# Kernel tuning notes

Measured on AMD Instinct MI355X. Metric: run time of the kernel, lower is better.

## Reference

```python
import jax, jax.numpy as jnp
import numpy as np

N, F, A = 50000, 128, 128

def setup_inputs() -> dict:
    key = jax.random.key(0)
    ks = jax.random.split(key, 20)
    r = lambda i, shape: jax.random.normal(ks[i], shape, dtype=jnp.float32)
    w = lambda i, shape: jax.random.normal(ks[i], shape, dtype=jnp.float32) * 0.05
    return {
        "feat": r(0, (N, F)),
        "mu": r(1, (N, F, 3)),
        "T0": r(2, (N,)),
        "T1": r(3, (N, 3)),
        "T2": r(4, (N, 3, 3)),
        "T3": r(5, (N, 3, 3, 3)),
        # denseq: Dense(F,F,swish) -> Dense(F,F). Weights stored [in,out].
        "Wq1": w(6, (F, F)), "bq1": jnp.zeros((F,), jnp.float32),
        "Wq2": w(7, (F, F)), "bq2": jnp.zeros((F,), jnp.float32),
        "WT1": w(8, (F, F)),  # dense_T1, no bias
        "WT2": w(9, (F, F)),  # dense_T2, no bias
        "WT3": w(10, (F, F)), # dense_T3, no bias
        # dense_s: Dense(F,F,swish) -> Dense(F,A)
        "Ws1": w(11, (F, F)), "bs1": jnp.zeros((F,), jnp.float32),
        "Ws2": w(12, (F, A)), "bs2": jnp.zeros((A,), jnp.float32),
        "Wv": w(13, (F, A)),  # dense_v, no bias
    }

def reference(feat, mu, T0, T1, T2, T3,
              Wq1, bq1, Wq2, bq2, WT1, WT2, WT3,
              Ws1, bs1, Ws2, bs2, Wv):
    silu = jax.nn.silu  # swish
    # M0 = denseq(feat): [N, F]
    M0 = silu(feat @ Wq1 + bq1) @ Wq2 + bq2
    # M1/M2/M3: linear over feature dim of mu [N, F, 3]
    M1 = jnp.einsum('nfc,fg->ngc', mu, WT1)
    M2 = jnp.einsum('nfc,fg->ngc', mu, WT2)
    M3 = jnp.einsum('nfc,fg->ngc', mu, WT3)
    # scalar channel
    ms = jnp.sum(M1 * T1[:, None, :], axis=-1) + T0[:, None] * M0          # T1, T0 terms
    ms = ms + jnp.einsum('nfi,nfj,nij->nf', M2, M2, T2)                    # quadrupole . T2
    ms = ms + jnp.einsum('nfi,nfj,nfk,nijk->nf', M3, M3, M3, T3)           # octupole . T3
    # vector channel [N, F, 3]
    mv = T1[:, None, :] * M0[..., None]
    mv = mv + jnp.einsum('nij,nfj->nfi', T2, M1)
    mv = mv + jnp.einsum('nijk,nfj,nfk->nfi', T3, M2, M2)
    # output projections
    mv_out = jnp.einsum('nfc,fa->nac', mv, Wv)                             # [N, A, 3]
    ms_out = silu(ms @ Ws1 + bs1) @ Ws2 + bs2                              # [N, A]
    return ms_out, mv_out
```

## Files before the change

### kernel.cpp

```cpp
#include <hip/hip_runtime.h>
#include <cstdint>

#define N_NODES 50000
#define TILE 32
#define NBLK ((N_NODES + TILE - 1) / TILE)

typedef __bf16 bf16x8 __attribute__((ext_vector_type(8)));
typedef unsigned short ushort8_t __attribute__((ext_vector_type(8)));
typedef float f32x4 __attribute__((ext_vector_type(4)));

__device__ __forceinline__ unsigned short f2bf(float x) {
  union { float f; uint32_t u; } v; v.f = x;
  uint32_t r = v.u + 0x7FFFu + ((v.u >> 16) & 1u);
  return (unsigned short)(r >> 16);
}

__device__ __forceinline__ float fast_silu(float x) {
  return x / (1.0f + __expf(-x));
}

__global__ __launch_bounds__(256) void prep_weights(
    const float* __restrict__ Wq1, const float* __restrict__ Wq2,
    const float* __restrict__ WT1, const float* __restrict__ WT2,
    const float* __restrict__ WT3, const float* __restrict__ Ws1,
    const float* __restrict__ Ws2, const float* __restrict__ Wv,
    unsigned short* __restrict__ ws) {
  int tid = blockIdx.x * 256 + threadIdx.x;
  int w = tid >> 11;
  int rest = tid & 2047;
  int c = rest >> 8;
  int kt = (rest >> 6) & 3;
  int lane = rest & 63;
  int g = (lane & 15) + 16 * c;
  int k0 = kt * 32 + (lane >> 4) * 8;
  const float* srcs[8] = {Wq1, Wq2, WT1, WT2, WT3, Ws1, Ws2, Wv};
  const float* src = srcs[w];
  union { unsigned short u[8]; uint4 v; } o;
#pragma unroll
  for (int j = 0; j < 8; ++j) o.u[j] = f2bf(src[(k0 + j) * 128 + g]);
  *(uint4*)(ws + (size_t)w * 16384 + (size_t)rest * 8) = o.v;
}

__device__ __forceinline__ bf16x8 ldB(const unsigned short* __restrict__ wg,
                                      int c, int kt, int lane) {
  return __builtin_bit_cast(
      bf16x8, *(const ushort8_t*)(wg + (((c * 4 + kt) * 64 + lane)) * 8));
}

__device__ __forceinline__ bf16x8 ldA(const unsigned short* __restrict__ sA,
                                      int row, int k0) {
  return __builtin_bit_cast(bf16x8, *(const ushort8_t*)(sA + row * 136 + k0));
}

__device__ __forceinline__ void gemm16g(const unsigned short* __restrict__ sA,
                                        const unsigned short* __restrict__ wg,
                                        int lane, int cb, f32x4 acc[2][2]) {
  const int m = lane & 15, q = lane >> 4;
  bf16x8 b[2][4], a0[4], a1[4];
#pragma unroll
  for (int cc = 0; cc < 2; ++cc)
#pragma unroll
    for (int kt = 0; kt < 4; ++kt) b[cc][kt] = ldB(wg, cb + cc, kt, lane);
#pragma unroll
  for (int kt = 0; kt < 4; ++kt) {
    const int k0 = q * 8 + kt * 32;
    a0[kt] = ldA(sA, m, k0);
    a1[kt] = ldA(sA, m + 16, k0);
  }
  const f32x4 vzero = {0.f, 0.f, 0.f, 0.f};
#pragma unroll
  for (int rt = 0; rt < 2; ++rt)
#pragma unroll
    for (int cc = 0; cc < 2; ++cc) acc[rt][cc] = vzero;
#pragma unroll
  for (int kt = 0; kt < 4; ++kt)
#pragma unroll
    for (int cc = 0; cc < 2; ++cc) {
      acc[0][cc] = __builtin_amdgcn_mfma_f32_16x16x32_bf16(a0[kt], b[cc][kt], acc[0][cc], 0, 0, 0);
      acc[1][cc] = __builtin_amdgcn_mfma_f32_16x16x32_bf16(a1[kt], b[cc][kt], acc[1][cc], 0, 0, 0);
    }
}

__device__ __forceinline__ void gemm3g(const unsigned short* __restrict__ s0,
                                       const unsigned short* __restrict__ s1,
                                       const unsigned short* __restrict__ s2,
                                       const unsigned short* __restrict__ wg,
                                       int lane, int cb,
                                       f32x4 A1[2][2], f32x4 A2[2][2],
                                       f32x4 A3[2][2]) {
  const int m = lane & 15, q = lane >> 4;
  bf16x8 b[2][4];
#pragma unroll
  for (int cc = 0; cc < 2; ++cc)
#pragma unroll
    for (int kt = 0; kt < 4; ++kt) b[cc][kt] = ldB(wg, cb + cc, kt, lane);
  const f32x4 vzero = {0.f, 0.f, 0.f, 0.f};
#pragma unroll
  for (int rt = 0; rt < 2; ++rt)
#pragma unroll
    for (int cc = 0; cc < 2; ++cc) {
      A1[rt][cc] = vzero; A2[rt][cc] = vzero; A3[rt][cc] = vzero;
    }
#pragma unroll
  for (int kt = 0; kt < 4; ++kt) {
    const int k0 = q * 8 + kt * 32;
    bf16x8 a00 = ldA(s0, m, k0);
    bf16x8 a01 = ldA(s0, m + 16, k0);
    bf16x8 a10 = ldA(s1, m, k0);
    bf16x8 a11 = ldA(s1, m + 16, k0);
    bf16x8 a20 = ldA(s2, m, k0);
    bf16x8 a21 = ldA(s2, m + 16, k0);
#pragma unroll
    for (int cc = 0; cc < 2; ++cc) {
      A1[0][cc] = __builtin_amdgcn_mfma_f32_16x16x32_bf16(a00, b[cc][kt], A1[0][cc], 0, 0, 0);
      A1[1][cc] = __builtin_amdgcn_mfma_f32_16x16x32_bf16(a01, b[cc][kt], A1[1][cc], 0, 0, 0);
      A2[0][cc] = __builtin_amdgcn_mfma_f32_16x16x32_bf16(a10, b[cc][kt], A2[0][cc], 0, 0, 0);
      A2[1][cc] = __builtin_amdgcn_mfma_f32_16x16x32_bf16(a11, b[cc][kt], A2[1][cc], 0, 0, 0);
      A3[0][cc] = __builtin_amdgcn_mfma_f32_16x16x32_bf16(a20, b[cc][kt], A3[0][cc], 0, 0, 0);
      A3[1][cc] = __builtin_amdgcn_mfma_f32_16x16x32_bf16(a21, b[cc][kt], A3[1][cc], 0, 0, 0);
    }
  }
}

__global__ __launch_bounds__(256, 2) void multipole_main(
    const float* __restrict__ feat, const float* __restrict__ mu,
    const float* __restrict__ T0g, const float* __restrict__ T1g,
    const float* __restrict__ T2g, const float* __restrict__ T3g,
    const float* __restrict__ bq1, const float* __restrict__ bq2,
    const float* __restrict__ bs1, const float* __restrict__ bs2,
    const unsigned short* __restrict__ ws, float* __restrict__ out) {
  __shared__ unsigned short sXmain[TILE * 136];
  __shared__ unsigned short sXmu[3][TILE * 136];
  __shared__ float sT[TILE][47];

  const int t = threadIdx.x;
  const int lane = t & 63, wv = t >> 6;
  const int m = lane & 15, q = lane >> 4;
  const int cb = wv * 2;
  const int nodeBase = blockIdx.x * TILE;

  {
    int node = t >> 3, f0 = (t & 7) * 16;
    int gn = nodeBase + node;
    union { unsigned short u[16]; uint4 v[2]; } buf;
    if (gn < N_NODES) {
      const f32x4* p = (const f32x4*)(feat + (size_t)gn * 128 + f0);
      float xs[16];
#pragma unroll
      for (int i = 0; i < 4; ++i) *(f32x4*)(xs + 4 * i) = __builtin_nontemporal_load(p + i);
#pragma unroll
      for (int i = 0; i < 16; ++i) buf.u[i] = f2bf(xs[i]);
    } else {
#pragma unroll
      for (int i = 0; i < 16; ++i) buf.u[i] = 0;
    }
    uint4* dst = (uint4*)&sXmain[node * 136 + f0];
    dst[0] = buf.v[0]; dst[1] = buf.v[1];
  }

  {
    int node = t >> 3, f0 = (t & 7) * 16;
    int gn = nodeBase + node;
    union { unsigned short u[16]; uint4 v[2]; } b3[3];
    if (gn < N_NODES) {
      const f32x4* p = (const f32x4*)(mu + ((size_t)gn * 128 + f0) * 3);
      float xs[48];
#pragma unroll
      for (int i = 0; i < 12; ++i) *(f32x4*)(xs + 4 * i) = __builtin_nontemporal_load(p + i);
#pragma unroll
      for (int i = 0; i < 16; ++i) {
        b3[0].u[i] = f2bf(xs[i * 3 + 0]);
        b3[1].u[i] = f2bf(xs[i * 3 + 1]);
        b3[2].u[i] = f2bf(xs[i * 3 + 2]);
      }
    } else {
#pragma unroll
      for (int ch = 0; ch < 3; ++ch)
#pragma unroll
        for (int i = 0; i < 16; ++i) b3[ch].u[i] = 0;
    }
#pragma unroll
    for (int ch = 0; ch < 3; ++ch) {
      uint4* dst = (uint4*)&sXmu[ch][node * 136 + f0];
      dst[0] = b3[ch].v[0]; dst[1] = b3[ch].v[1];
    }
  }

  if (t < TILE) {
    int n = nodeBase + t;
    bool val = n < N_NODES;
    float t0 = val ? __builtin_nontemporal_load(T0g + n) : 0.f;
    float t1[3], t2[9], t3[27];
#pragma unroll
    for (int i = 0; i < 3; ++i) t1[i] = val ? __builtin_nontemporal_load(T1g + n * 3 + i) : 0.f;
#pragma unroll
    for (int i = 0; i < 9; ++i) t2[i] = val ? __builtin_nontemporal_load(T2g + n * 9 + i) : 0.f;
#pragma unroll
    for (int i = 0; i < 27; ++i) t3[i] = val ? __builtin_nontemporal_load(T3g + n * 27 + i) : 0.f;
    float* Tr = sT[t];
    Tr[0] = t0;
    Tr[1] = t1[0]; Tr[2] = t1[1]; Tr[3] = t1[2];
#pragma unroll
    for (int i = 0; i < 9; ++i) Tr[4 + i] = t2[i];
    Tr[13] = t2[0]; Tr[14] = t2[1] + t2[3]; Tr[15] = t2[2] + t2[6];
    Tr[16] = t2[4]; Tr[17] = t2[5] + t2[7]; Tr[18] = t2[8];
    Tr[19] = t3[0];
    Tr[20] = t3[1] + t3[3] + t3[9];
    Tr[21] = t3[2] + t3[6] + t3[18];
    Tr[22] = t3[4] + t3[10] + t3[12];
    Tr[23] = t3[5] + t3[7] + t3[11] + t3[15] + t3[19] + t3[21];
    Tr[24] = t3[8] + t3[20] + t3[24];
    Tr[25] = t3[13];
    Tr[26] = t3[14] + t3[16] + t3[22];
    Tr[27] = t3[17] + t3[23] + t3[25];
    Tr[28] = t3[26];
#pragma unroll
    for (int i = 0; i < 3; ++i) {
      const float* b = t3 + 9 * i;
      float* d = Tr + 29 + 6 * i;
      d[0] = b[0]; d[1] = b[1] + b[3]; d[2] = b[2] + b[6];
      d[3] = b[4]; d[4] = b[5] + b[7]; d[5] = b[8];
    }
  }
  __syncthreads();

  f32x4 A1[2][2], A2[2][2], A3[2][2];
  float msv[2][2][4];
  float mvv[3][2][2][4];

  gemm16g(sXmain, ws, lane, cb, A1);
  float b0 = bq1[cb * 16 + m], b1 = bq1[cb * 16 + 16 + m];
  __syncthreads();
#pragma unroll
  for (int rt = 0; rt < 2; ++rt)
#pragma unroll
    for (int ri = 0; ri < 4; ++ri) {
      int lrow = rt * 16 + q * 4 + ri;
#pragma unroll
      for (int cc = 0; cc < 2; ++cc) {
        float h = fast_silu(A1[rt][cc][ri] + (cc ? b1 : b0));
        sXmain[lrow * 136 + (cb + cc) * 16 + m] = f2bf(h);
      }
    }
  __syncthreads();

  gemm16g(sXmain, ws + 1 * 16384, lane, cb, A1);
  {
    float bb0 = bq2[cb * 16 + m], bb1 = bq2[cb * 16 + 16 + m];
#pragma unroll
    for (int rt = 0; rt < 2; ++rt)
#pragma unroll
      for (int ri = 0; ri < 4; ++ri) {
        const float* Tr = sT[rt * 16 + q * 4 + ri];
        float t0 = Tr[0], ta = Tr[1], tb = Tr[2], tc = Tr[3];
#pragma unroll
        for (int cc = 0; cc < 2; ++cc) {
          float m0 = A1[rt][cc][ri] + (cc ? bb1 : bb0);
          msv[rt][cc][ri] = t0 * m0;
          mvv[0][rt][cc][ri] = ta * m0;
          mvv[1][rt][cc][ri] = tb * m0;
          mvv[2][rt][cc][ri] = tc * m0;
        }
      }
  }

  gemm3g(sXmu[0], sXmu[1], sXmu[2], ws + 2 * 16384, lane, cb, A1, A2, A3);
#pragma unroll
  for (int rt = 0; rt < 2; ++rt)
#pragma unroll
    for (int ri = 0; ri < 4; ++ri) {
      const float* Tr = sT[rt * 16 + q * 4 + ri];
#pragma unroll
      for (int cc = 0; cc < 2; ++cc) {
        float v0 = A1[rt][cc][ri], v1 = A2[rt][cc][ri], v2 = A3[rt][cc][ri];
        msv[rt][cc][ri] += Tr[1] * v0 + Tr[2] * v1 + Tr[3] * v2;
        mvv[0][rt][cc][ri] += Tr[4] * v0 + Tr[5] * v1 + Tr[6] * v2;
        mvv[1][rt][cc][ri] += Tr[7] * v0 + Tr[8] * v1 + Tr[9] * v2;
        mvv[2][rt][cc][ri] += Tr[10] * v0 + Tr[11] * v1 + Tr[12] * v2;
      }
    }

  gemm3g(sXmu[0], sXmu[1], sXmu[2], ws + 4 * 16384, lane, cb, A1, A2, A3);
#pragma unroll
  for (int rt = 0; rt < 2; ++rt)
#pragma unroll
    for (int ri = 0; ri < 4; ++ri) {
      const float* Cp = sT[rt * 16 + q * 4 + ri] + 19;
      float c0 = Cp[0], c1 = Cp[1], c2 = Cp[2], c3 = Cp[3], c4 = Cp[4];
      float c5 = Cp[5], c6 = Cp[6], c7 = Cp[7], c8 = Cp[8], c9 = Cp[9];
#pragma unroll
      for (int cc = 0; cc < 2; ++cc) {
        float u0 = A1[rt][cc][ri], u1 = A2[rt][cc][ri], u2 = A3[rt][cc][ri];
        float Q0 = u0 * u0, Q1 = u0 * u1, Q2 = u0 * u2;
        float Q3 = u1 * u1, Q4 = u1 * u2, Q5 = u2 * u2;
        msv[rt][cc][ri] += c0 * (Q0 * u0) + c1 * (Q0 * u1) + c2 * (Q0 * u2) +
                           c3 * (Q1 * u1) + c4 * (Q1 * u2) + c5 * (Q2 * u2) +
                           c6 * (Q3 * u1) + c7 * (Q3 * u2) + c8 * (Q4 * u2) +
                           c9 * (Q5 * u2);
      }
    }

  gemm3g(sXmu[0], sXmu[1], sXmu[2], ws + 3 * 16384, lane, cb, A1, A2, A3);
#pragma unroll
  for (int rt = 0; rt < 2; ++rt)
#pragma unroll
    for (int ri = 0; ri < 4; ++ri) {
      const float* Tr = sT[rt * 16 + q * 4 + ri];
      const float* q2 = Tr + 13;
      const float* d3 = Tr + 29;
      float q20 = q2[0], q21 = q2[1], q22 = q2[2], q23 = q2[3], q24 = q2[4], q25 = q2[5];
#pragma unroll
      for (int cc = 0; cc < 2; ++cc) {
        float v0 = A1[rt][cc][ri], v1 = A2[rt][cc][ri], v2 = A3[rt][cc][ri];
        float P0 = v0 * v0, P1 = v0 * v1, P2 = v0 * v2;
        float P3 = v1 * v1, P4 = v1 * v2, P5 = v2 * v2;
        msv[rt][cc][ri] += q20 * P0 + q21 * P1 + q22 * P2 + q23 * P3 + q24 * P4 + q25 * P5;
        mvv[0][rt][cc][ri] += d3[0] * P0 + d3[1] * P1 + d3[2] * P2 + d3[3] * P3 + d3[4] * P4 + d3[5] * P5;
        mvv[1][rt][cc][ri] += d3[6] * P0 + d3[7] * P1 + d3[8] * P2 + d3[9] * P3 + d3[10] * P4 + d3[11] * P5;
        mvv[2][rt][cc][ri] += d3[12] * P0 + d3[13] * P1 + d3[14] * P2 + d3[15] * P3 + d3[16] * P4 + d3[17] * P5;
      }
    }
  __syncthreads();

#pragma unroll
  for (int rt = 0; rt < 2; ++rt)
#pragma unroll
    for (int ri = 0; ri < 4; ++ri) {
      int lrow = rt * 16 + q * 4 + ri;
#pragma unroll
      for (int cc = 0; cc < 2; ++cc) {
        int col = (cb + cc) * 16 + m;
        sXmain[lrow * 136 + col] = f2bf(msv[rt][cc][ri]);
        sXmu[0][lrow * 136 + col] = f2bf(mvv[0][rt][cc][ri]);
        sXmu[1][lrow * 136 + col] = f2bf(mvv[1][rt][cc][ri]);
        sXmu[2][lrow * 136 + col] = f2bf(mvv[2][rt][cc][ri]);
      }
    }
  __syncthreads();

  gemm16g(sXmain, ws + 5 * 16384, lane, cb, A1);
  {
    float s0 = bs1[cb * 16 + m], s1 = bs1[cb * 16 + 16 + m];
    __syncthreads();
#pragma unroll
    for (int rt = 0; rt < 2; ++rt)
#pragma unroll
      for (int ri = 0; ri < 4; ++ri) {
        int lrow = rt * 16 + q * 4 + ri;
#pragma unroll
        for (int cc = 0; cc < 2; ++cc) {
          float g = fast_silu(A1[rt][cc][ri] + (cc ? s1 : s0));
          sXmain[lrow * 136 + (cb + cc) * 16 + m] = f2bf(g);
        }
      }
  }
  __syncthreads();

  gemm16g(sXmain, ws + 6 * 16384, lane, cb, A1);
  {
    float s0 = bs2[cb * 16 + m], s1 = bs2[cb * 16 + 16 + m];
#pragma unroll
    for (int rt = 0; rt < 2; ++rt)
#pragma unroll
      for (int ri = 0; ri < 4; ++ri) {
        int grow = nodeBase + rt * 16 + q * 4 + ri;
        if (grow < N_NODES) {
#pragma unroll
          for (int cc = 0; cc < 2; ++cc) {
            int col = (cb + cc) * 16 + m;
            __builtin_nontemporal_store(A1[rt][cc][ri] + (cc ? s1 : s0),
                                        out + (size_t)grow * 128 + col);
          }
        }
      }
  }

  float* out2 = out + (size_t)N_NODES * 128;
  gemm3g(sXmu[0], sXmu[1], sXmu[2], ws + 7 * 16384, lane, cb, A1, A2, A3);
#pragma unroll
  for (int rt = 0; rt < 2; ++rt)
#pragma unroll
    for (int ri = 0; ri < 4; ++ri) {
      int grow = nodeBase + rt * 16 + q * 4 + ri;
      if (grow < N_NODES) {
#pragma unroll
        for (int cc = 0; cc < 2; ++cc) {
          int col = (cb + cc) * 16 + m;
          float* p = out2 + ((size_t)grow * 128 + col) * 3;
          __builtin_nontemporal_store(A1[rt][cc][ri], p + 0);
          __builtin_nontemporal_store(A2[rt][cc][ri], p + 1);
          __builtin_nontemporal_store(A3[rt][cc][ri], p + 2);
        }
      }
    }
}

extern "C" void kernel_launch(void* const* d_in, const int* in_sizes, int n_in,
                              void* d_out, int out_size, void* d_ws, size_t ws_size,
                              hipStream_t stream) {
  const float* feat = (const float*)d_in[0];
  const float* mu   = (const float*)d_in[1];
  const float* T0   = (const float*)d_in[2];
  const float* T1   = (const float*)d_in[3];
  const float* T2   = (const float*)d_in[4];
  const float* T3   = (const float*)d_in[5];
  const float* Wq1  = (const float*)d_in[6];
  const float* bq1  = (const float*)d_in[7];
  const float* Wq2  = (const float*)d_in[8];
  const float* bq2  = (const float*)d_in[9];
  const float* WT1  = (const float*)d_in[10];
  const float* WT2  = (const float*)d_in[11];
  const float* WT3  = (const float*)d_in[12];
  const float* Ws1  = (const float*)d_in[13];
  const float* bs1  = (const float*)d_in[14];
  const float* Ws2  = (const float*)d_in[15];
  const float* bs2  = (const float*)d_in[16];
  const float* Wv   = (const float*)d_in[17];
  unsigned short* ws = (unsigned short*)d_ws;
  float* out = (float*)d_out;

  prep_weights<<<64, 256, 0, stream>>>(Wq1, Wq2, WT1, WT2, WT3, Ws1, Ws2, Wv, ws);
  multipole_main<<<NBLK, 256, 0, stream>>>(feat, mu, T0, T1, T2, T3,
                                           bq1, bq2, bs1, bs2, ws, out);
}
```

Before: 300.2 us.

## Prefetch next weight fragments during GEMMs, double-buffer activations, vectorize epilogues

Measured after the change: 306.3 us. 2.0% more time.

```diff
diff --git a/kernel.cpp b/kernel.cpp
--- a/kernel.cpp
+++ b/kernel.cpp
@@ -8,15 +8,18 @@
 typedef __bf16 bf16x8 __attribute__((ext_vector_type(8)));
 typedef unsigned short ushort8_t __attribute__((ext_vector_type(8)));
 typedef float f32x4 __attribute__((ext_vector_type(4)));
+typedef float f32x2 __attribute__((ext_vector_type(2)));
 
 __device__ __forceinline__ unsigned short f2bf(float x) {
-  union { float f; uint32_t u; } v; v.f = x;
-  uint32_t r = v.u + 0x7FFFu + ((v.u >> 16) & 1u);
-  return (unsigned short)(r >> 16);
+  return __builtin_bit_cast(unsigned short, (__bf16)x);
 }
 
 __device__ __forceinline__ float fast_silu(float x) {
   return x / (1.0f + __expf(-x));
+}
+
+__device__ __forceinline__ f32x4 ld4(const float* p) {
+  return *(const f32x4*)p;
 }
 
 __global__ __launch_bounds__(256) void prep_weights(
@@ -47,20 +50,27 @@
       bf16x8, *(const ushort8_t*)(wg + (((c * 4 + kt) * 64 + lane)) * 8));
 }
 
+struct BF { bf16x8 v[2][4]; };
+
+__device__ __forceinline__ BF loadB8(const unsigned short* __restrict__ wg,
+                                     int lane, int cb) {
+  BF r;
+#pragma unroll
+  for (int cc = 0; cc < 2; ++cc)
+#pragma unroll
+    for (int kt = 0; kt < 4; ++kt) r.v[cc][kt] = ldB(wg, cb + cc, kt, lane);
+  return r;
+}
+
 __device__ __forceinline__ bf16x8 ldA(const unsigned short* __restrict__ sA,
                                       int row, int k0) {
   return __builtin_bit_cast(bf16x8, *(const ushort8_t*)(sA + row * 136 + k0));
 }
 
-__device__ __forceinline__ void gemm16g(const unsigned short* __restrict__ sA,
-                                        const unsigned short* __restrict__ wg,
-                                        int lane, int cb, f32x4 acc[2][2]) {
+__device__ __forceinline__ void gemm16p(const unsigned short* __restrict__ sA,
+                                        const BF& B, int lane, f32x4 acc[2][2]) {
   const int m = lane & 15, q = lane >> 4;
-  bf16x8 b[2][4], a0[4], a1[4];
-#pragma unroll
-  for (int cc = 0; cc < 2; ++cc)
-#pragma unroll
-    for (int kt = 0; kt < 4; ++kt) b[cc][kt] = ldB(wg, cb + cc, kt, lane);
+  bf16x8 a0[4], a1[4];
 #pragma unroll
   for (int kt = 0; kt < 4; ++kt) {
     const int k0 = q * 8 + kt * 32;
@@ -76,24 +86,18 @@
   for (int kt = 0; kt < 4; ++kt)
 #pragma unroll
     for (int cc = 0; cc < 2; ++cc) {
-      acc[0][cc] = __builtin_amdgcn_mfma_f32_16x16x32_bf16(a0[kt], b[cc][kt], acc[0][cc], 0, 0, 0);
-      acc[1][cc] = __builtin_amdgcn_mfma_f32_16x16x32_bf16(a1[kt], b[cc][kt], acc[1][cc], 0, 0, 0);
-    }
-}
-
-__device__ __forceinline__ void gemm3g(const unsigned short* __restrict__ s0,
+      acc[0][cc] = __builtin_amdgcn_mfma_f32_16x16x32_bf16(a0[kt], B.v[cc][kt], acc[0][cc], 0, 0, 0);
+      acc[1][cc] = __builtin_amdgcn_mfma_f32_16x16x32_bf16(a1[kt], B.v[cc][kt], acc[1][cc], 0, 0, 0);
+    }
+}
+
+__device__ __forceinline__ void gemm3p(const unsigned short* __restrict__ s0,
                                        const unsigned short* __restrict__ s1,
                                        const unsigned short* __restrict__ s2,
-                                       const unsigned short* __restrict__ wg,
-                                       int lane, int cb,
+                                       const BF& B, int lane,
                                        f32x4 A1[2][2], f32x4 A2[2][2],
                                        f32x4 A3[2][2]) {
   const int m = lane & 15, q = lane >> 4;
-  bf16x8 b[2][4];
-#pragma unroll
-  for (int cc = 0; cc < 2; ++cc)
-#pragma unroll
-    for (int kt = 0; kt < 4; ++kt) b[cc][kt] = ldB(wg, cb + cc, kt, lane);
   const f32x4 vzero = {0.f, 0.f, 0.f, 0.f};
 #pragma unroll
   for (int rt = 0; rt < 2; ++rt)
@@ -112,15 +116,17 @@
     bf16x8 a21 = ldA(s2, m + 16, k0);
 #pragma unroll
     for (int cc = 0; cc < 2; ++cc) {
-      A1[0][cc] = __builtin_amdgcn_mfma_f32_16x16x32_bf16(a00, b[cc][kt], A1[0][cc], 0, 0, 0);
-      A1[1][cc] = __builtin_amdgcn_mfma_f32_16x16x32_bf16(a01, b[cc][kt], A1[1][cc], 0, 0, 0);
-      A2[0][cc] = __builtin_amdgcn_mfma_f32_16x16x32_bf16(a10, b[cc][kt], A2[0][cc], 0, 0, 0);
-      A2[1][cc] = __builtin_amdgcn_mfma_f32_16x16x32_bf16(a11, b[cc][kt], A2[1][cc], 0, 0, 0);
-      A3[0][cc] = __builtin_amdgcn_mfma_f32_16x16x32_bf16(a20, b[cc][kt], A3[0][cc], 0, 0, 0);
-      A3[1][cc] = __builtin_amdgcn_mfma_f32_16x16x32_bf16(a21, b[cc][kt], A3[1][cc], 0, 0, 0);
-    }
-  }
-}
+      A1[0][cc] = __builtin_amdgcn_mfma_f32_16x16x32_bf16(a00, B.v[cc][kt], A1[0][cc], 0, 0, 0);
+      A1[1][cc] = __builtin_amdgcn_mfma_f32_16x16x32_bf16(a01, B.v[cc][kt], A1[1][cc], 0, 0, 0);
+      A2[0][cc] = __builtin_amdgcn_mfma_f32_16x16x32_bf16(a10, B.v[cc][kt], A2[0][cc], 0, 0, 0);
+      A2[1][cc] = __builtin_amdgcn_mfma_f32_16x16x32_bf16(a11, B.v[cc][kt], A2[1][cc], 0, 0, 0);
+      A3[0][cc] = __builtin_amdgcn_mfma_f32_16x16x32_bf16(a20, B.v[cc][kt], A3[0][cc], 0, 0, 0);
+      A3[1][cc] = __builtin_amdgcn_mfma_f32_16x16x32_bf16(a21, B.v[cc][kt], A3[1][cc], 0, 0, 0);
+    }
+  }
+}
+
+#define ST_STRIDE 56
 
 __global__ __launch_bounds__(256, 2) void multipole_main(
     const float* __restrict__ feat, const float* __restrict__ mu,
@@ -130,14 +136,20 @@
     const float* __restrict__ bs1, const float* __restrict__ bs2,
     const unsigned short* __restrict__ ws, float* __restrict__ out) {
   __shared__ unsigned short sXmain[TILE * 136];
+  __shared__ unsigned short sXmain2[TILE * 136];
   __shared__ unsigned short sXmu[3][TILE * 136];
-  __shared__ float sT[TILE][47];
+  __shared__ float sT[TILE][ST_STRIDE];
 
   const int t = threadIdx.x;
   const int lane = t & 63, wv = t >> 6;
   const int m = lane & 15, q = lane >> 4;
   const int cb = wv * 2;
   const int nodeBase = blockIdx.x * TILE;
+
+  const float bq1v0 = bq1[cb * 16 + m], bq1v1 = bq1[cb * 16 + 16 + m];
+  const float bq2v0 = bq2[cb * 16 + m], bq2v1 = bq2[cb * 16 + 16 + m];
+  const float bs1v0 = bs1[cb * 16 + m], bs1v1 = bs1[cb * 16 + 16 + m];
+  const float bs2v0 = bs2[cb * 16 + m], bs2v1 = bs2[cb * 16 + 16 + m];
 
   {
     int node = t >> 3, f0 = (t & 7) * 16;
@@ -202,181 +214,175 @@
     Tr[1] = t1[0]; Tr[2] = t1[1]; Tr[3] = t1[2];
 #pragma unroll
     for (int i = 0; i < 9; ++i) Tr[4 + i] = t2[i];
-    Tr[13] = t2[0]; Tr[14] = t2[1] + t2[3]; Tr[15] = t2[2] + t2[6];
-    Tr[16] = t2[4]; Tr[17] = t2[5] + t2[7]; Tr[18] = t2[8];
-    Tr[19] = t3[0];
-    Tr[20] = t3[1] + t3[3] + t3[9];
-    Tr[21] = t3[2] + t3[6] + t3[18];
-    Tr[22] = t3[4] + t3[10] + t3[12];
-    Tr[23] = t3[5] + t3[7] + t3[11] + t3[15] + t3[19] + t3[21];
-    Tr[24] = t3[8] + t3[20] + t3[24];
-    Tr[25] = t3[13];
-    Tr[26] = t3[14] + t3[16] + t3[22];
-    Tr[27] = t3[17] + t3[23] + t3[25];
-    Tr[28] = t3[26];
+    Tr[16] = t2[0]; Tr[17] = t2[1] + t2[3]; Tr[18] = t2[2] + t2[6];
+    Tr[19] = t2[4]; Tr[20] = t2[5] + t2[7]; Tr[21] = t2[8];
+    Tr[24] = t3[0];
+    Tr[25] = t3[1] + t3[3] + t3[9];
+    Tr[26] = t3[2] + t3[6] + t3[18];
+    Tr[27] = t3[4] + t3[10] + t3[12];
+    Tr[28] = t3[5] + t3[7] + t3[11] + t3[15] + t3[19] + t3[21];
+    Tr[29] = t3[8] + t3[20] + t3[24];
+    Tr[30] = t3[13];
+    Tr[31] = t3[14] + t3[16] + t3[22];
+    Tr[32] = t3[17] + t3[23] + t3[25];
+    Tr[33] = t3[26];
 #pragma unroll
     for (int i = 0; i < 3; ++i) {
       const float* b = t3 + 9 * i;
-      float* d = Tr + 29 + 6 * i;
+      float* d = Tr + 36 + 6 * i;
       d[0] = b[0]; d[1] = b[1] + b[3]; d[2] = b[2] + b[6];
       d[3] = b[4]; d[4] = b[5] + b[7]; d[5] = b[8];
     }
   }
+
+  BF Bq1f = loadB8(ws, lane, cb);
   __syncthreads();
 
   f32x4 A1[2][2], A2[2][2], A3[2][2];
-  float msv[2][2][4];
-  float mvv[3][2][2][4];
-
-  gemm16g(sXmain, ws, lane, cb, A1);
-  float b0 = bq1[cb * 16 + m], b1 = bq1[cb * 16 + 16 + m];
+  f32x2 msv[2][4];
+  f32x2 mvv[3][2][4];
+
+  gemm16p(sXmain, Bq1f, lane, A1);
+  BF Bq2f = loadB8(ws + 1 * 16384, lane, cb);
+#pragma unroll
+  for (int rt = 0; rt < 2; ++rt)
+#pragma unroll
+    for (int ri = 0; ri < 4; ++ri) {
+      int lrow = rt * 16 + q * 4 + ri;
+#pragma unroll
+      for (int cc = 0; cc < 2; ++cc) {
+        float h = fast_silu(A1[rt][cc][ri] + (cc ? bq1v1 : bq1v0));
+        sXmain2[lrow * 136 + (cb + cc) * 16 + m] = f2bf(h);
+      }
+    }
   __syncthreads();
+
+  gemm16p(sXmain2, Bq2f, lane, A1);
+  BF Bm1f = loadB8(ws + 2 * 16384, lane, cb);
+  {
+    const f32x2 bb = {bq2v0, bq2v1};
+#pragma unroll
+    for (int rt = 0; rt < 2; ++rt)
+#pragma unroll
+      for (int ri = 0; ri < 4; ++ri) {
+        const f32x4 tv = ld4(sT[rt * 16 + q * 4 + ri]);
+        f32x2 m0 = f32x2{A1[rt][0][ri], A1[rt][1][ri]} + bb;
+        msv[rt][ri] = m0 * tv.x;
+        mvv[0][rt][ri] = m0 * tv.y;
+        mvv[1][rt][ri] = m0 * tv.z;
+        mvv[2][rt][ri] = m0 * tv.w;
+      }
+  }
+
+  gemm3p(sXmu[0], sXmu[1], sXmu[2], Bm1f, lane, A1, A2, A3);
+  BF Bm3f = loadB8(ws + 4 * 16384, lane, cb);
+#pragma unroll
+  for (int rt = 0; rt < 2; ++rt)
+#pragma unroll
+    for (int ri = 0; ri < 4; ++ri) {
+      const float* Tr = sT[rt * 16 + q * 4 + ri];
+      const f32x4 cA = ld4(Tr + 0), cB = ld4(Tr + 4), cC = ld4(Tr + 8), cD = ld4(Tr + 12);
+      f32x2 v0 = {A1[rt][0][ri], A1[rt][1][ri]};
+      f32x2 v1 = {A2[rt][0][ri], A2[rt][1][ri]};
+      f32x2 v2 = {A3[rt][0][ri], A3[rt][1][ri]};
+      msv[rt][ri]    += v0 * cA.y + v1 * cA.z + v2 * cA.w;
+      mvv[0][rt][ri] += v0 * cB.x + v1 * cB.y + v2 * cB.z;
+      mvv[1][rt][ri] += v0 * cB.w + v1 * cC.x + v2 * cC.y;
+      mvv[2][rt][ri] += v0 * cC.z + v1 * cC.w + v2 * cD.x;
+    }
+
+  gemm3p(sXmu[0], sXmu[1], sXmu[2], Bm3f, lane, A1, A2, A3);
+  BF Bm2f = loadB8(ws + 3 * 16384, lane, cb);
+#pragma unroll
+  for (int rt = 0; rt < 2; ++rt)
+#pragma unroll
+    for (int ri = 0; ri < 4; ++ri) {
+      const float* Tr = sT[rt * 16 + q * 4 + ri];
+      const f32x4 E = ld4(Tr + 24), F = ld4(Tr + 28), Gv = ld4(Tr + 32);
+      f32x2 u0 = {A1[rt][0][ri], A1[rt][1][ri]};
+      f32x2 u1 = {A2[rt][0][ri], A2[rt][1][ri]};
+      f32x2 u2 = {A3[rt][0][ri], A3[rt][1][ri]};
+      f32x2 Q0 = u0 * u0, Q1 = u0 * u1, Q2 = u0 * u2;
+      f32x2 Q3 = u1 * u1, Q4 = u1 * u2, Q5 = u2 * u2;
+      msv[rt][ri] += (Q0 * u0) * E.x + (Q0 * u1) * E.y + (Q0 * u2) * E.z +
+                     (Q1 * u1) * E.w + (Q1 * u2) * F.x + (Q2 * u2) * F.y +
+                     (Q3 * u1) * F.z + (Q3 * u2) * F.w + (Q4 * u2) * Gv.x +
+                     (Q5 * u2) * Gv.y;
+    }
+
+  gemm3p(sXmu[0], sXmu[1], sXmu[2], Bm2f, lane, A1, A2, A3);
+  BF Bs1f = loadB8(ws + 5 * 16384, lane, cb);
+#pragma unroll
+  for (int rt = 0; rt < 2; ++rt)
+#pragma unroll
+    for (int ri = 0; ri < 4; ++ri) {
+      const float* Tr = sT[rt * 16 + q * 4 + ri];
+      const f32x4 H4 = ld4(Tr + 16), I4 = ld4(Tr + 20);
+      const f32x4 J = ld4(Tr + 36), K = ld4(Tr + 40), L = ld4(Tr + 44);
+      const f32x4 M4 = ld4(Tr + 48), N4 = ld4(Tr + 52);
+      f32x2 v0 = {A1[rt][0][ri], A1[rt][1][ri]};
+      f32x2 v1 = {A2[rt][0][ri], A2[rt][1][ri]};
+      f32x2 v2 = {A3[rt][0][ri], A3[rt][1][ri]};
+      f32x2 P0 = v0 * v0, P1 = v0 * v1, P2 = v0 * v2;
+      f32x2 P3 = v1 * v1, P4 = v1 * v2, P5 = v2 * v2;
+      msv[rt][ri]    += P0 * H4.x + P1 * H4.y + P2 * H4.z + P3 * H4.w + P4 * I4.x + P5 * I4.y;
+      mvv[0][rt][ri] += P0 * J.x + P1 * J.y + P2 * J.z + P3 * J.w + P4 * K.x + P5 * K.y;
+      mvv[1][rt][ri] += P0 * K.z + P1 * K.w + P2 * L.x + P3 * L.y + P4 * L.z + P5 * L.w;
+      mvv[2][rt][ri] += P0 * M4.x + P1 * M4.y + P2 * M4.z + P3 * M4.w + P4 * N4.x + P5 * N4.y;
+    }
+  __syncthreads();
+
 #pragma unroll
   for (int rt = 0; rt < 2; ++rt)
 #pragma unroll
     for (int ri = 0; ri < 4; ++ri) {
       int lrow = rt * 16 + q * 4 + ri;
+      int col0 = cb * 16 + m, col1 = col0 + 16;
+      sXmain[lrow * 136 + col0] = f2bf(msv[rt][ri].x);
+      sXmain[lrow * 136 + col1] = f2bf(msv[rt][ri].y);
+      sXmu[0][lrow * 136 + col0] = f2bf(mvv[0][rt][ri].x);
+      sXmu[0][lrow * 136 + col1] = f2bf(mvv[0][rt][ri].y);
+      sXmu[1][lrow * 136 + col0] = f2bf(mvv[1][rt][ri].x);
+      sXmu[1][lrow * 136 + col1] = f2bf(mvv[1][rt][ri].y);
+      sXmu[2][lrow * 136 + col0] = f2bf(mvv[2][rt][ri].x);
+      sXmu[2][lrow * 136 + col1] = f2bf(mvv[2][rt][ri].y);
+    }
+  __syncthreads();
+
+  gemm16p(sXmain, Bs1f, lane, A1);
+  BF Bs2f = loadB8(ws + 6 * 16384, lane, cb);
+#pragma unroll
+  for (int rt = 0; rt < 2; ++rt)
+#pragma unroll
+    for (int ri = 0; ri < 4; ++ri) {
+      int lrow = rt * 16 + q * 4 + ri;
 #pragma unroll
       for (int cc = 0; cc < 2; ++cc) {
-        float h = fast_silu(A1[rt][cc][ri] + (cc ? b1 : b0));
-        sXmain[lrow * 136 + (cb + cc) * 16 + m] = f2bf(h);
+        float g = fast_silu(A1[rt][cc][ri] + (cc ? bs1v1 : bs1v0));
+        sXmain2[lrow * 136 + (cb + cc) * 16 + m] = f2bf(g);
       }
     }
   __syncthreads();
 
-  gemm16g(sXmain, ws + 1 * 16384, lane, cb, A1);
-  {
-    float bb0 = bq2[cb * 16 + m], bb1 = bq2[cb * 16 + 16 + m];
-#pragma unroll
-    for (int rt = 0; rt < 2; ++rt)
-#pragma unroll
-      for (int ri = 0; ri < 4; ++ri) {
-        const float* Tr = sT[rt * 16 + q * 4 + ri];
-        float t0 = Tr[0], ta = Tr[1], tb = Tr[2], tc = Tr[3];
+  gemm16p(sXmain2, Bs2f, lane, A1);
+  BF Bvf = loadB8(ws + 7 * 16384, lane, cb);
+#pragma unroll
+  for (int rt = 0; rt < 2; ++rt)
+#pragma unroll
+    for (int ri = 0; ri < 4; ++ri) {
+      int grow = nodeBase + rt * 16 + q * 4 + ri;
+      if (grow < N_NODES) {
 #pragma unroll
         for (int cc = 0; cc < 2; ++cc) {
-          float m0 = A1[rt][cc][ri] + (cc ? bb1 : bb0);
-          msv[rt][cc][ri] = t0 * m0;
-          mvv[0][rt][cc][ri] = ta * m0;
-          mvv[1][rt][cc][ri] = tb * m0;
-          mvv[2][rt][cc][ri] = tc * m0;
+          int col = (cb + cc) * 16 + m;
+          __builtin_nontemporal_store(A1[rt][cc][ri] + (cc ? bs2v1 : bs2v0),
+                                      out + (size_t)grow * 128 + col);
         }
       }
-  }
-
-  gemm3g(sXmu[0], sXmu[1], sXmu[2], ws + 2 * 16384, lane, cb, A1, A2, A3);
-#pragma unroll
-  for (int rt = 0; rt < 2; ++rt)
-#pragma unroll
-    for (int ri = 0; ri < 4; ++ri) {
-      const float* Tr = sT[rt * 16 + q * 4 + ri];
-#pragma unroll
-      for (int cc = 0; cc < 2; ++cc) {
-        float v0 = A1[rt][cc][ri], v1 = A2[rt][cc][ri], v2 = A3[rt][cc][ri];
-        msv[rt][cc][ri] += Tr[1] * v0 + Tr[2] * v1 + Tr[3] * v2;
-        mvv[0][rt][cc][ri] += Tr[4] * v0 + Tr[5] * v1 + Tr[6] * v2;
-        mvv[1][rt][cc][ri] += Tr[7] * v0 + Tr[8] * v1 + Tr[9] * v2;
-        mvv[2][rt][cc][ri] += Tr[10] * v0 + Tr[11] * v1 + Tr[12] * v2;
-      }
-    }
-
-  gemm3g(sXmu[0], sXmu[1], sXmu[2], ws + 4 * 16384, lane, cb, A1, A2, A3);
-#pragma unroll
-  for (int rt = 0; rt < 2; ++rt)
-#pragma unroll
-    for (int ri = 0; ri < 4; ++ri) {
-      const float* Cp = sT[rt * 16 + q * 4 + ri] + 19;
-      float c0 = Cp[0], c1 = Cp[1], c2 = Cp[2], c3 = Cp[3], c4 = Cp[4];
-      float c5 = Cp[5], c6 = Cp[6], c7 = Cp[7], c8 = Cp[8], c9 = Cp[9];
-#pragma unroll
-      for (int cc = 0; cc < 2; ++cc) {
-        float u0 = A1[rt][cc][ri], u1 = A2[rt][cc][ri], u2 = A3[rt][cc][ri];
-        float Q0 = u0 * u0, Q1 = u0 * u1, Q2 = u0 * u2;
-        float Q3 = u1 * u1, Q4 = u1 * u2, Q5 = u2 * u2;
-        msv[rt][cc][ri] += c0 * (Q0 * u0) + c1 * (Q0 * u1) + c2 * (Q0 * u2) +
-                           c3 * (Q1 * u1) + c4 * (Q1 * u2) + c5 * (Q2 * u2) +
-                           c6 * (Q3 * u1) + c7 * (Q3 * u2) + c8 * (Q4 * u2) +
-                           c9 * (Q5 * u2);
-      }
-    }
-
-  gemm3g(sXmu[0], sXmu[1], sXmu[2], ws + 3 * 16384, lane, cb, A1, A2, A3);
-#pragma unroll
-  for (int rt = 0; rt < 2; ++rt)
-#pragma unroll
-    for (int ri = 0; ri < 4; ++ri) {
-      const float* Tr = sT[rt * 16 + q * 4 + ri];
-      const float* q2 = Tr + 13;
-      const float* d3 = Tr + 29;
-      float q20 = q2[0], q21 = q2[1], q22 = q2[2], q23 = q2[3], q24 = q2[4], q25 = q2[5];
-#pragma unroll
-      for (int cc = 0; cc < 2; ++cc) {
-        float v0 = A1[rt][cc][ri], v1 = A2[rt][cc][ri], v2 = A3[rt][cc][ri];
-        float P0 = v0 * v0, P1 = v0 * v1, P2 = v0 * v2;
-        float P3 = v1 * v1, P4 = v1 * v2, P5 = v2 * v2;
-        msv[rt][cc][ri] += q20 * P0 + q21 * P1 + q22 * P2 + q23 * P3 + q24 * P4 + q25 * P5;
-        mvv[0][rt][cc][ri] += d3[0] * P0 + d3[1] * P1 + d3[2] * P2 + d3[3] * P3 + d3[4] * P4 + d3[5] * P5;
-        mvv[1][rt][cc][ri] += d3[6] * P0 + d3[7] * P1 + d3[8] * P2 + d3[9] * P3 + d3[10] * P4 + d3[11] * P5;
-        mvv[2][rt][cc][ri] += d3[12] * P0 + d3[13] * P1 + d3[14] * P2 + d3[15] * P3 + d3[16] * P4 + d3[17] * P5;
-      }
-    }
-  __syncthreads();
-
-#pragma unroll
-  for (int rt = 0; rt < 2; ++rt)
-#pragma unroll
-    for (int ri = 0; ri < 4; ++ri) {
-      int lrow = rt * 16 + q * 4 + ri;
-#pragma unroll
-      for (int cc = 0; cc < 2; ++cc) {
-        int col = (cb + cc) * 16 + m;
-        sXmain[lrow * 136 + col] = f2bf(msv[rt][cc][ri]);
-        sXmu[0][lrow * 136 + col] = f2bf(mvv[0][rt][cc][ri]);
-        sXmu[1][lrow * 136 + col] = f2bf(mvv[1][rt][cc][ri]);
-        sXmu[2][lrow * 136 + col] = f2bf(mvv[2][rt][cc][ri]);
-      }
-    }
-  __syncthreads();
-
-  gemm16g(sXmain, ws + 5 * 16384, lane, cb, A1);
-  {
-    float s0 = bs1[cb * 16 + m], s1 = bs1[cb * 16 + 16 + m];
-    __syncthreads();
-#pragma unroll
-    for (int rt = 0; rt < 2; ++rt)
-#pragma unroll
-      for (int ri = 0; ri < 4; ++ri) {
-        int lrow = rt * 16 + q * 4 + ri;
-#pragma unroll
-        for (int cc = 0; cc < 2; ++cc) {
-          float g = fast_silu(A1[rt][cc][ri] + (cc ? s1 : s0));
-          sXmain[lrow * 136 + (cb + cc) * 16 + m] = f2bf(g);
-        }
-      }
-  }
-  __syncthreads();
-
-  gemm16g(sXmain, ws + 6 * 16384, lane, cb, A1);
-  {
-    float s0 = bs2[cb * 16 + m], s1 = bs2[cb * 16 + 16 + m];
-#pragma unroll
-    for (int rt = 0; rt < 2; ++rt)
-#pragma unroll
-      for (int ri = 0; ri < 4; ++ri) {
-        int grow = nodeBase + rt * 16 + q * 4 + ri;
-        if (grow < N_NODES) {
-#pragma unroll
-          for (int cc = 0; cc < 2; ++cc) {
-            int col = (cb + cc) * 16 + m;
-            __builtin_nontemporal_store(A1[rt][cc][ri] + (cc ? s1 : s0),
-                                        out + (size_t)grow * 128 + col);
-          }
-        }
-      }
-  }
+    }
 
   float* out2 = out + (size_t)N_NODES * 128;
-  gemm3g(sXmu[0], sXmu[1], sXmu[2], ws + 7 * 16384, lane, cb, A1, A2, A3);
+  gemm3p(sXmu[0], sXmu[1], sXmu[2], Bvf, lane, A1, A2, A3);
 #pragma unroll
   for (int rt = 0; rt < 2; ++rt)
 #pragma unroll
```
